# Performance work log

Hardware: AMD Instinct MI355X
Metric: run time of the kernel (lower is better)

## Reference

```python
import jax, jax.numpy as jnp
import numpy as np
import math

SEQ_LEN, PRED_LEN, CHANNELS, RANK = 720, 336, 862, 32
IN_LEN = SEQ_LEN // 2  # Haar low-pass with stride 2 (seq_len even)
BATCH = 256


def _dct2_ortho_mat(N):
    # D[k, n] = s_k * 2 * cos(pi * k * (2n+1) / (2N)); orthonormal DCT-II
    k = np.arange(N)[:, None]
    n = np.arange(N)[None, :]
    D = 2.0 * np.cos(np.pi * k * (2 * n + 1) / (2 * N))
    s = np.full(N, np.sqrt(1.0 / (2 * N)))
    s[0] = np.sqrt(1.0 / (4 * N))
    return jnp.asarray((s[:, None] * D).astype(np.float32))


def _idct2_unnorm_mat(N):
    # scipy.fft.idct(type=2, norm=None): out[n] = (1/N) * (x0/2 + sum_{k>=1} x_k cos(pi k (2n+1)/(2N)))
    # Returned as M[k, n] so that out = x @ M along last axis.
    k = np.arange(N)[:, None]
    n = np.arange(N)[None, :]
    M = np.cos(np.pi * k * (2 * n + 1) / (2 * N)) / N
    M[0, :] *= 0.5
    return jnp.asarray(M.astype(np.float32))


D_DCT = _dct2_ortho_mat(IN_LEN)        # [IN_LEN, IN_LEN]
M_IDCT = _idct2_unnorm_mat(PRED_LEN)   # [PRED_LEN, PRED_LEN]
INV_SQRT2 = 1.0 / math.sqrt(2.0)


def setup_inputs() -> dict:
    key = jax.random.key(0)
    k1, k2, k3, k4 = jax.random.split(key, 4)
    x = jax.random.normal(k1, (BATCH, SEQ_LEN, CHANNELS), dtype=jnp.float32)
    # kaiming_uniform-like scales for LowRank params
    boundA = math.sqrt(6.0 / IN_LEN)
    boundB = math.sqrt(6.0 / RANK)
    A = jax.random.uniform(k2, (IN_LEN, RANK), dtype=jnp.float32, minval=-boundA, maxval=boundA)
    B = jax.random.uniform(k3, (RANK, PRED_LEN), dtype=jnp.float32, minval=-boundB, maxval=boundB)
    b = jax.random.uniform(k4, (PRED_LEN,), dtype=jnp.float32)
    return {"x": x, "A": A, "B": B, "b": b}


def reference(x, A, B, b):
    # x: [B, L, C] -> [B, C, L]
    xt = jnp.transpose(x, (0, 2, 1))
    seq_mean = jnp.mean(xt, axis=-1, keepdims=True)          # [B, C, 1]
    xc = xt - seq_mean
    # Haar low-pass: depthwise conv1d with [1,1]/sqrt(2), stride 2
    h = (xc[..., ::2] + xc[..., 1::2]) * INV_SQRT2           # [B, C, IN_LEN]
    # orthonormal DCT-II along last axis, then divide by length
    y = jnp.einsum('bcn,kn->bck', h, D_DCT) / IN_LEN         # [B, C, IN_LEN]
    # low-rank prediction head (shared across channels)
    z = (y @ A) @ B + b                                      # [B, C, PRED_LEN]
    # unnormalized inverse DCT-II (scipy idct type=2, norm=None)
    o = z @ M_IDCT                                           # [B, C, PRED_LEN]
    o = o + seq_mean
    return jnp.transpose(o, (0, 2, 1))                       # [B, PRED_LEN, C]
```

## Files before the change

kernel.cpp:

```cpp
#include <hip/hip_runtime.h>
#include <math.h>

#define SEQ_LEN   720
#define IN_LEN    360
#define PRED_LEN  336
#define CHANNELS  862
#define RANK      32
#define BATCH     256

typedef _Float16 h2 __attribute__((ext_vector_type(2)));

#define WS_WP    0
#define WS_VT    11520
#define WS_CVEC  22272
#define WS_WH    22608
#define WS_VH    28368

__device__ __forceinline__ float fdot2w(h2 a, h2 b, float c) {
#if __has_builtin(__builtin_amdgcn_fdot2)
    return __builtin_amdgcn_fdot2(a, b, c, false);
#else
    return fmaf((float)a[0], (float)b[0], fmaf((float)a[1], (float)b[1], c));
#endif
}
__device__ __forceinline__ h2 pkrtz(float a, float b) {
    return __builtin_bit_cast(h2, __builtin_amdgcn_cvt_pkrtz(a, b));
}
#define BC(u) __builtin_bit_cast(h2, (u))

__global__ __launch_bounds__(256) void k_prep(const float* __restrict__ A,
                                              const float* __restrict__ B,
                                              const float* __restrict__ bias,
                                              float* __restrict__ Wp,
                                              float* __restrict__ Vt,
                                              float* __restrict__ cvec) {
    __shared__ float sbuf[IN_LEN * RANK];
    int blk = blockIdx.x;
    if (blk < 45) {
        for (int i = threadIdx.x; i < IN_LEN * RANK; i += 256) sbuf[i] = A[i];
        __syncthreads();
        int idx = blk * 256 + threadIdx.x;
        int n = idx >> 5, r = idx & 31;
        int step = 2 * n + 1, m = 0;
        float sum = 0.f;
        for (int k = 0; k < IN_LEN; ++k) {
            float coef = (k == 0) ? 0.05270462766947299f
                                  : 0.07453559924999299f;
            float d = coef * cospif((float)m * (1.0f / 720.0f));
            sum = fmaf(d, sbuf[k * RANK + r], sum);
            m += step; if (m >= 1440) m -= 1440;
        }
        Wp[idx] = sum * 0.0019641855032960957f;
    } else if (blk < 87) {
        for (int i = threadIdx.x; i < PRED_LEN * RANK; i += 256) {
            int r = i / PRED_LEN, k = i - r * PRED_LEN;
            sbuf[k * RANK + r] = B[i];
        }
        __syncthreads();
        int idx = (blk - 45) * 256 + threadIdx.x;
        int n = idx >> 5, r = idx & 31;
        int step = 2 * n + 1, m = 0;
        float sum = 0.f;
        for (int k = 0; k < PRED_LEN; ++k) {
            float mk = cospif((float)m * (1.0f / 672.0f));
            if (k == 0) mk *= 0.5f;
            sum = fmaf(mk, sbuf[k * RANK + r], sum);
            m += step; if (m >= 1344) m -= 1344;
        }
        Vt[idx] = sum * (1.0f / 336.0f);
    } else {
        int n = (blk - 87) * 256 + threadIdx.x;
        if (n < PRED_LEN) {
            int step = 2 * n + 1, m = 0;
            float sum = 0.f;
            for (int k = 0; k < PRED_LEN; ++k) {
                float mk = cospif((float)m * (1.0f / 672.0f));
                if (k == 0) mk *= 0.5f;
                sum = fmaf(mk, bias[k], sum);
                m += step; if (m >= 1344) m -= 1344;
            }
            cvec[n] = sum * (1.0f / 336.0f);
        }
    }
}

__global__ __launch_bounds__(256) void k_pack(const float* __restrict__ Wp,
                                              const float* __restrict__ Vt,
                                              unsigned* __restrict__ Wh,
                                              unsigned* __restrict__ Vh) {
    int idx = blockIdx.x * 256 + threadIdx.x;
    if (idx < 5760) {
        int np = idx >> 5, r = idx & 31;
        h2 v = pkrtz(Wp[(2 * np) * RANK + r], Wp[(2 * np + 1) * RANK + r]);
        Wh[idx] = __builtin_bit_cast(unsigned, v);
    } else if (idx < 5760 + 5376) {
        int j = idx - 5760;
        int n = j >> 4, q = j & 15;
        h2 v = pkrtz(Vt[n * RANK + 2 * q], Vt[n * RANK + 2 * q + 1]);
        Vh[j] = __builtin_bit_cast(unsigned, v);
    }
}

__global__ __launch_bounds__(256) void k_main(const float* __restrict__ x,
                                              const float* __restrict__ A,
                                              const unsigned* __restrict__ Wh,
                                              const unsigned* __restrict__ Vh,
                                              const float* __restrict__ cvec,
                                              float* __restrict__ out) {
    __shared__ uint4 lds4[1440];
    unsigned* ldsu = (unsigned*)lds4;
    const int tid = threadIdx.x;
    const int b = blockIdx.y;
    const int c = blockIdx.x * 256 + tid;
    const bool active = (c < CHANNELS);

    {
        const uint4* s = (const uint4*)Wh;
        for (int i = tid; i < 1440; i += 256) lds4[i] = s[i];
    }
    __syncthreads();

    float acc[RANK];
    #pragma unroll
    for (int r = 0; r < RANK; ++r) acc[r] = 0.f;
    float S = 0.f, mean = 0.f;
    h2 th[16];

    if (active) {
        const float* xp = x + (size_t)b * (SEQ_LEN * CHANNELS) + c;

        float bufA[8], bufB[8];
        #define LOADB(BUF, BD) { const float* p_ = xp + (size_t)(BD) * (8 * CHANNELS); \
            _Pragma("unroll") \
            for (int j_ = 0; j_ < 8; ++j_) BUF[j_] = p_[j_ * CHANNELS]; }

        #define NPBODY(BUF, S_) { \
            float pe = BUF[4*S_+0] + BUF[4*S_+1]; \
            float po = BUF[4*S_+2] + BUF[4*S_+3]; \
            S += pe + po; \
            h2 P = pkrtz(pe, po); \
            _Pragma("unroll") \
            for (int q_ = 0; q_ < 8; ++q_) { \
                uint4 wv = wr[8*S_ + q_]; \
                acc[4*q_+0] = fdot2w(P, BC(wv.x), acc[4*q_+0]); \
                acc[4*q_+1] = fdot2w(P, BC(wv.y), acc[4*q_+1]); \
                acc[4*q_+2] = fdot2w(P, BC(wv.z), acc[4*q_+2]); \
                acc[4*q_+3] = fdot2w(P, BC(wv.w), acc[4*q_+3]); \
            } }

        #define BODY(BUF, BD) { const uint4* wr = lds4 + 16 * (BD); \
            NPBODY(BUF, 0); NPBODY(BUF, 1); }

        LOADB(bufA, 0)
        for (int it = 0; it < 45; ++it) {
            LOADB(bufB, 2 * it + 1)
            BODY(bufA, 2 * it)
            if (it < 44) LOADB(bufA, 2 * it + 2)
            BODY(bufB, 2 * it + 1)
        }
        #undef BODY
        #undef NPBODY
        #undef LOADB

        const float k360 = (1.0f / 360.0f) * 0.037267799624996496f;
        float g = -S * k360;
        #pragma unroll
        for (int q = 0; q < 8; ++q) {
            float4 a4 = ((const float4*)A)[q];
            acc[4*q+0] = fmaf(g, a4.x, acc[4*q+0]);
            acc[4*q+1] = fmaf(g, a4.y, acc[4*q+1]);
            acc[4*q+2] = fmaf(g, a4.z, acc[4*q+2]);
            acc[4*q+3] = fmaf(g, a4.w, acc[4*q+3]);
        }
        mean = S * (1.0f / 720.0f);

        #pragma unroll
        for (int u = 0; u < 16; ++u) th[u] = pkrtz(acc[2*u], acc[2*u+1]);
    }
    __syncthreads();

    {
        const uint4* s = (const uint4*)Vh;
        for (int i = tid; i < 1344; i += 256) lds4[i] = s[i];
        for (int i = tid; i < PRED_LEN; i += 256)
            ldsu[5376 + i] = __float_as_uint(cvec[i]);
    }
    __syncthreads();

    if (active) {
        float* op = out + (size_t)b * (PRED_LEN * CHANNELS) + c;
        #pragma unroll 2
        for (int n = 0; n < PRED_LEN; ++n) {
            const uint4* vr = lds4 + n * 4;
            float oA = 0.f, oB = 0.f;
            #pragma unroll
            for (int q = 0; q < 4; ++q) {
                uint4 v = vr[q];
                oA = fdot2w(th[4*q+0], BC(v.x), oA);
                oB = fdot2w(th[4*q+1], BC(v.y), oB);
                oA = fdot2w(th[4*q+2], BC(v.z), oA);
                oB = fdot2w(th[4*q+3], BC(v.w), oB);
            }
            float cvn = __uint_as_float(ldsu[5376 + n]);
            *op = (oA + oB) + cvn + mean;
            op += CHANNELS;
        }
    }
}


extern "C" void kernel_launch(void* const* d_in, const int* in_sizes, int n_in,
                              void* d_out, int out_size, void* d_ws, size_t ws_size,
                              hipStream_t stream) {
    (void)in_sizes; (void)n_in; (void)out_size; (void)ws_size;
    const float* x    = (const float*)d_in[0];
    const float* A    = (const float*)d_in[1];
    const float* B    = (const float*)d_in[2];
    const float* bias = (const float*)d_in[3];
    float* out = (float*)d_out;
    float* ws  = (float*)d_ws;

    float*    Wp   = ws + WS_WP;
    float*    Vt   = ws + WS_VT;
    float*    cvec = ws + WS_CVEC;
    unsigned* Wh   = (unsigned*)(ws + WS_WH);
    unsigned* Vh   = (unsigned*)(ws + WS_VH);

    k_prep<<<dim3(89), dim3(256), 0, stream>>>(A, B, bias, Wp, Vt, cvec);
    k_pack<<<dim3(44), dim3(256), 0, stream>>>(Wp, Vt, Wh, Vh);
    k_main<<<dim3(4, BATCH), dim3(256), 0, stream>>>(x, A, Wh, Vh, cvec, out);
}
```

Measured before the change: 309.8 us.

## Process four channels per thread with packed-half FMA and split sequence halves

Restructures k_main so each of 512 threads handles four adjacent channels with float2 loads, and the two thread halves split the time axis in the projection phase and the output axis in the reconstruction phase. Partial accumulators are exchanged through LDS. Accumulation now uses packed fp16 FMA with fp16 accumulators instead of fdot2 into fp32, which raises throughput but risks precision loss over 180 accumulations. One block now covers a whole batch, with W, V and cvec staged in LDS once, cutting grid size and LDS reload overhead.

After: 271.6 us. -12.3%, faster.

```diff
diff --git a/kernel.cpp b/kernel.cpp
--- a/kernel.cpp
+++ b/kernel.cpp
@@ -16,6 +16,11 @@
 #define WS_WH    22608
 #define WS_VH    28368
 
+#define L_EX     0
+#define L_W      29376
+#define L_V      35136
+#define L_CV     40512
+
 __device__ __forceinline__ float fdot2w(h2 a, h2 b, float c) {
 #if __has_builtin(__builtin_amdgcn_fdot2)
     return __builtin_amdgcn_fdot2(a, b, c, false);
@@ -26,7 +31,8 @@
 __device__ __forceinline__ h2 pkrtz(float a, float b) {
     return __builtin_bit_cast(h2, __builtin_amdgcn_cvt_pkrtz(a, b));
 }
-#define BC(u) __builtin_bit_cast(h2, (u))
+#define BC(u)  __builtin_bit_cast(h2, (u))
+#define BCU(v) __builtin_bit_cast(unsigned, (v))
 
 __global__ __launch_bounds__(256) void k_prep(const float* __restrict__ A,
                                               const float* __restrict__ B,
@@ -90,119 +96,189 @@
                                               unsigned* __restrict__ Vh) {
     int idx = blockIdx.x * 256 + threadIdx.x;
     if (idx < 5760) {
-        int np = idx >> 5, r = idx & 31;
-        h2 v = pkrtz(Wp[(2 * np) * RANK + r], Wp[(2 * np + 1) * RANK + r]);
-        Wh[idx] = __builtin_bit_cast(unsigned, v);
+        int n = idx >> 4, j = idx & 15;
+        h2 v = pkrtz(Wp[n * RANK + 2 * j], Wp[n * RANK + 2 * j + 1]);
+        Wh[idx] = BCU(v);
     } else if (idx < 5760 + 5376) {
-        int j = idx - 5760;
-        int n = j >> 4, q = j & 15;
-        h2 v = pkrtz(Vt[n * RANK + 2 * q], Vt[n * RANK + 2 * q + 1]);
-        Vh[j] = __builtin_bit_cast(unsigned, v);
-    }
-}
-
-__global__ __launch_bounds__(256) void k_main(const float* __restrict__ x,
+        int k = idx - 5760;
+        int n = k >> 4, j = k & 15;
+        h2 v = pkrtz(Vt[n * RANK + 2 * j], Vt[n * RANK + 2 * j + 1]);
+        Vh[k] = BCU(v);
+    }
+}
+
+__global__ __launch_bounds__(512) void k_main(const float* __restrict__ x,
                                               const float* __restrict__ A,
                                               const unsigned* __restrict__ Wh,
                                               const unsigned* __restrict__ Vh,
                                               const float* __restrict__ cvec,
                                               float* __restrict__ out) {
-    __shared__ uint4 lds4[1440];
-    unsigned* ldsu = (unsigned*)lds4;
+    __shared__ unsigned ldsu[40848];
     const int tid = threadIdx.x;
-    const int b = blockIdx.y;
-    const int c = blockIdx.x * 256 + tid;
-    const bool active = (c < CHANNELS);
-
-    {
-        const uint4* s = (const uint4*)Wh;
-        for (int i = tid; i < 1440; i += 256) lds4[i] = s[i];
-    }
+    const int b = blockIdx.x;
+    const int h = tid >> 8;
+    const int i = tid & 255;
+    const bool active = (i < 216);
+    const int c0 = (i < 215) ? 4 * i : 858;
+
+    for (int idx = tid; idx < 1440; idx += 512)
+        ((uint4*)(ldsu + L_W))[idx] = ((const uint4*)Wh)[idx];
+    for (int idx = tid; idx < 1344; idx += 512)
+        ((uint4*)(ldsu + L_V))[idx] = ((const uint4*)Vh)[idx];
+    for (int idx = tid; idx < 84; idx += 512)
+        ((uint4*)(ldsu + L_CV))[idx] = ((const uint4*)cvec)[idx];
     __syncthreads();
 
-    float acc[RANK];
+    h2 acc0[16], acc1[16], acc2[16], acc3[16];
     #pragma unroll
-    for (int r = 0; r < RANK; ++r) acc[r] = 0.f;
-    float S = 0.f, mean = 0.f;
-    h2 th[16];
+    for (int j = 0; j < 16; ++j) {
+        acc0[j] = pkrtz(0.f, 0.f); acc1[j] = pkrtz(0.f, 0.f);
+        acc2[j] = pkrtz(0.f, 0.f); acc3[j] = pkrtz(0.f, 0.f);
+    }
+    float S0 = 0.f, S1 = 0.f, S2 = 0.f, S3 = 0.f;
 
     if (active) {
-        const float* xp = x + (size_t)b * (SEQ_LEN * CHANNELS) + c;
-
-        float bufA[8], bufB[8];
-        #define LOADB(BUF, BD) { const float* p_ = xp + (size_t)(BD) * (8 * CHANNELS); \
+        const float* xp = x + (size_t)b * (SEQ_LEN * CHANNELS)
+                            + (size_t)h * (IN_LEN * CHANNELS) + c0;
+        float2 bA[4], bB[4];
+        #define LOADN(BUF, NL) { const float* p_ = xp + (size_t)(2 * (NL)) * CHANNELS; \
+            BUF[0] = *(const float2*)(p_);                 \
+            BUF[1] = *(const float2*)(p_ + 2);             \
+            BUF[2] = *(const float2*)(p_ + CHANNELS);      \
+            BUF[3] = *(const float2*)(p_ + CHANNELS + 2); }
+
+        #define BODY(BUF, NL) { \
+            float p0 = BUF[0].x + BUF[2].x; \
+            float p1 = BUF[0].y + BUF[2].y; \
+            float p2 = BUF[1].x + BUF[3].x; \
+            float p3 = BUF[1].y + BUF[3].y; \
+            S0 += p0; S1 += p1; S2 += p2; S3 += p3; \
+            h2 P0 = pkrtz(p0, p0), P1 = pkrtz(p1, p1); \
+            h2 P2 = pkrtz(p2, p2), P3 = pkrtz(p3, p3); \
+            const uint4* wr = (const uint4*)(ldsu + L_W) + ((NL) + 180 * h) * 4; \
             _Pragma("unroll") \
-            for (int j_ = 0; j_ < 8; ++j_) BUF[j_] = p_[j_ * CHANNELS]; }
-
-        #define NPBODY(BUF, S_) { \
-            float pe = BUF[4*S_+0] + BUF[4*S_+1]; \
-            float po = BUF[4*S_+2] + BUF[4*S_+3]; \
-            S += pe + po; \
-            h2 P = pkrtz(pe, po); \
-            _Pragma("unroll") \
-            for (int q_ = 0; q_ < 8; ++q_) { \
-                uint4 wv = wr[8*S_ + q_]; \
-                acc[4*q_+0] = fdot2w(P, BC(wv.x), acc[4*q_+0]); \
-                acc[4*q_+1] = fdot2w(P, BC(wv.y), acc[4*q_+1]); \
-                acc[4*q_+2] = fdot2w(P, BC(wv.z), acc[4*q_+2]); \
-                acc[4*q_+3] = fdot2w(P, BC(wv.w), acc[4*q_+3]); \
+            for (int q_ = 0; q_ < 4; ++q_) { \
+                uint4 wv = wr[q_]; \
+                h2 w0 = BC(wv.x), w1 = BC(wv.y), w2 = BC(wv.z), w3 = BC(wv.w); \
+                acc0[4*q_+0] = w0 * P0 + acc0[4*q_+0]; \
+                acc1[4*q_+0] = w0 * P1 + acc1[4*q_+0]; \
+                acc2[4*q_+0] = w0 * P2 + acc2[4*q_+0]; \
+                acc3[4*q_+0] = w0 * P3 + acc3[4*q_+0]; \
+                acc0[4*q_+1] = w1 * P0 + acc0[4*q_+1]; \
+                acc1[4*q_+1] = w1 * P1 + acc1[4*q_+1]; \
+                acc2[4*q_+1] = w1 * P2 + acc2[4*q_+1]; \
+                acc3[4*q_+1] = w1 * P3 + acc3[4*q_+1]; \
+                acc0[4*q_+2] = w2 * P0 + acc0[4*q_+2]; \
+                acc1[4*q_+2] = w2 * P1 + acc1[4*q_+2]; \
+                acc2[4*q_+2] = w2 * P2 + acc2[4*q_+2]; \
+                acc3[4*q_+2] = w2 * P3 + acc3[4*q_+2]; \
+                acc0[4*q_+3] = w3 * P0 + acc0[4*q_+3]; \
+                acc1[4*q_+3] = w3 * P1 + acc1[4*q_+3]; \
+                acc2[4*q_+3] = w3 * P2 + acc2[4*q_+3]; \
+                acc3[4*q_+3] = w3 * P3 + acc3[4*q_+3]; \
             } }
 
-        #define BODY(BUF, BD) { const uint4* wr = lds4 + 16 * (BD); \
-            NPBODY(BUF, 0); NPBODY(BUF, 1); }
-
-        LOADB(bufA, 0)
-        for (int it = 0; it < 45; ++it) {
-            LOADB(bufB, 2 * it + 1)
-            BODY(bufA, 2 * it)
-            if (it < 44) LOADB(bufA, 2 * it + 2)
-            BODY(bufB, 2 * it + 1)
+        LOADN(bA, 0)
+        for (int n = 0; n < 180; n += 2) {
+            LOADN(bB, n + 1)
+            BODY(bA, n)
+            if (n + 2 < 180) LOADN(bA, n + 2)
+            BODY(bB, n + 1)
         }
         #undef BODY
-        #undef NPBODY
-        #undef LOADB
-
-        const float k360 = (1.0f / 360.0f) * 0.037267799624996496f;
-        float g = -S * k360;
+        #undef LOADN
+    }
+
+    if (active) {
+        uint4* rec = (uint4*)(ldsu + (i + 216 * h) * 68);
+        #pragma unroll
+        for (int q = 0; q < 4; ++q) {
+            uint4 v;
+            v.x = BCU(acc0[4*q+0]); v.y = BCU(acc0[4*q+1]);
+            v.z = BCU(acc0[4*q+2]); v.w = BCU(acc0[4*q+3]);
+            rec[q] = v;
+            v.x = BCU(acc1[4*q+0]); v.y = BCU(acc1[4*q+1]);
+            v.z = BCU(acc1[4*q+2]); v.w = BCU(acc1[4*q+3]);
+            rec[4 + q] = v;
+            v.x = BCU(acc2[4*q+0]); v.y = BCU(acc2[4*q+1]);
+            v.z = BCU(acc2[4*q+2]); v.w = BCU(acc2[4*q+3]);
+            rec[8 + q] = v;
+            v.x = BCU(acc3[4*q+0]); v.y = BCU(acc3[4*q+1]);
+            v.z = BCU(acc3[4*q+2]); v.w = BCU(acc3[4*q+3]);
+            rec[12 + q] = v;
+        }
+        uint4 sv;
+        sv.x = __float_as_uint(S0); sv.y = __float_as_uint(S1);
+        sv.z = __float_as_uint(S2); sv.w = __float_as_uint(S3);
+        rec[16] = sv;
+    }
+    __syncthreads();
+
+    float mean0 = 0.f, mean1 = 0.f, mean2 = 0.f, mean3 = 0.f;
+    if (active) {
+        const uint4* pr = (const uint4*)(ldsu + (i + 216 * (1 - h)) * 68);
+        #pragma unroll
+        for (int q = 0; q < 4; ++q) {
+            uint4 v = pr[q];
+            acc0[4*q+0] = acc0[4*q+0] + BC(v.x); acc0[4*q+1] = acc0[4*q+1] + BC(v.y);
+            acc0[4*q+2] = acc0[4*q+2] + BC(v.z); acc0[4*q+3] = acc0[4*q+3] + BC(v.w);
+            v = pr[4 + q];
+            acc1[4*q+0] = acc1[4*q+0] + BC(v.x); acc1[4*q+1] = acc1[4*q+1] + BC(v.y);
+            acc1[4*q+2] = acc1[4*q+2] + BC(v.z); acc1[4*q+3] = acc1[4*q+3] + BC(v.w);
+            v = pr[8 + q];
+            acc2[4*q+0] = acc2[4*q+0] + BC(v.x); acc2[4*q+1] = acc2[4*q+1] + BC(v.y);
+            acc2[4*q+2] = acc2[4*q+2] + BC(v.z); acc2[4*q+3] = acc2[4*q+3] + BC(v.w);
+            v = pr[12 + q];
+            acc3[4*q+0] = acc3[4*q+0] + BC(v.x); acc3[4*q+1] = acc3[4*q+1] + BC(v.y);
+            acc3[4*q+2] = acc3[4*q+2] + BC(v.z); acc3[4*q+3] = acc3[4*q+3] + BC(v.w);
+        }
+        uint4 sv = pr[16];
+        S0 += __uint_as_float(sv.x); S1 += __uint_as_float(sv.y);
+        S2 += __uint_as_float(sv.z); S3 += __uint_as_float(sv.w);
+
+        const float kc = (1.0f / 360.0f) * 0.037267799624996496f;
+        float g0 = -S0 * kc, g1 = -S1 * kc, g2 = -S2 * kc, g3 = -S3 * kc;
+        h2 G0 = pkrtz(g0, g0), G1 = pkrtz(g1, g1), G2 = pkrtz(g2, g2), G3 = pkrtz(g3, g3);
         #pragma unroll
         for (int q = 0; q < 8; ++q) {
             float4 a4 = ((const float4*)A)[q];
-            acc[4*q+0] = fmaf(g, a4.x, acc[4*q+0]);
-            acc[4*q+1] = fmaf(g, a4.y, acc[4*q+1]);
-            acc[4*q+2] = fmaf(g, a4.z, acc[4*q+2]);
-            acc[4*q+3] = fmaf(g, a4.w, acc[4*q+3]);
-        }
-        mean = S * (1.0f / 720.0f);
-
-        #pragma unroll
-        for (int u = 0; u < 16; ++u) th[u] = pkrtz(acc[2*u], acc[2*u+1]);
-    }
-    __syncthreads();
-
-    {
-        const uint4* s = (const uint4*)Vh;
-        for (int i = tid; i < 1344; i += 256) lds4[i] = s[i];
-        for (int i = tid; i < PRED_LEN; i += 256)
-            ldsu[5376 + i] = __float_as_uint(cvec[i]);
-    }
-    __syncthreads();
-
-    if (active) {
-        float* op = out + (size_t)b * (PRED_LEN * CHANNELS) + c;
-        #pragma unroll 2
-        for (int n = 0; n < PRED_LEN; ++n) {
-            const uint4* vr = lds4 + n * 4;
-            float oA = 0.f, oB = 0.f;
+            h2 aa = pkrtz(a4.x, a4.y), ab = pkrtz(a4.z, a4.w);
+            acc0[2*q]   = aa * G0 + acc0[2*q];   acc0[2*q+1] = ab * G0 + acc0[2*q+1];
+            acc1[2*q]   = aa * G1 + acc1[2*q];   acc1[2*q+1] = ab * G1 + acc1[2*q+1];
+            acc2[2*q]   = aa * G2 + acc2[2*q];   acc2[2*q+1] = ab * G2 + acc2[2*q+1];
+            acc3[2*q]   = aa * G3 + acc3[2*q];   acc3[2*q+1] = ab * G3 + acc3[2*q+1];
+        }
+        mean0 = S0 * (1.0f / 720.0f); mean1 = S1 * (1.0f / 720.0f);
+        mean2 = S2 * (1.0f / 720.0f); mean3 = S3 * (1.0f / 720.0f);
+
+        float* op = out + (size_t)b * (PRED_LEN * CHANNELS)
+                        + (size_t)(168 * h) * CHANNELS + c0;
+        for (int nl = 0; nl < 168; ++nl) {
+            const int n = 168 * h + nl;
+            const uint4* vr = (const uint4*)(ldsu + L_V) + n * 4;
+            float o0 = 0.f, o1 = 0.f, o2 = 0.f, o3 = 0.f;
+            float e0 = 0.f, e1 = 0.f, e2 = 0.f, e3 = 0.f;
             #pragma unroll
             for (int q = 0; q < 4; ++q) {
                 uint4 v = vr[q];
-                oA = fdot2w(th[4*q+0], BC(v.x), oA);
-                oB = fdot2w(th[4*q+1], BC(v.y), oB);
-                oA = fdot2w(th[4*q+2], BC(v.z), oA);
-                oB = fdot2w(th[4*q+3], BC(v.w), oB);
+                h2 v0 = BC(v.x), v1 = BC(v.y), v2 = BC(v.z), v3 = BC(v.w);
+                o0 = fdot2w(acc0[4*q+0], v0, o0); e0 = fdot2w(acc0[4*q+1], v1, e0);
+                o1 = fdot2w(acc1[4*q+0], v0, o1); e1 = fdot2w(acc1[4*q+1], v1, e1);
+                o2 = fdot2w(acc2[4*q+0], v0, o2); e2 = fdot2w(acc2[4*q+1], v1, e2);
+                o3 = fdot2w(acc3[4*q+0], v0, o3); e3 = fdot2w(acc3[4*q+1], v1, e3);
+                o0 = fdot2w(acc0[4*q+2], v2, o0); e0 = fdot2w(acc0[4*q+3], v3, e0);
+                o1 = fdot2w(acc1[4*q+2], v2, o1); e1 = fdot2w(acc1[4*q+3], v3, e1);
+                o2 = fdot2w(acc2[4*q+2], v2, o2); e2 = fdot2w(acc2[4*q+3], v3, e2);
+                o3 = fdot2w(acc3[4*q+2], v2, o3); e3 = fdot2w(acc3[4*q+3], v3, e3);
             }
-            float cvn = __uint_as_float(ldsu[5376 + n]);
-            *op = (oA + oB) + cvn + mean;
+            float cvn = ((const float*)(ldsu + L_CV))[n];
+            float2 w0, w1;
+            w0.x = (o0 + e0) + cvn + mean0;
+            w0.y = (o1 + e1) + cvn + mean1;
+            w1.x = (o2 + e2) + cvn + mean2;
+            w1.y = (o3 + e3) + cvn + mean3;
+            *(float2*)(op)     = w0;
+            *(float2*)(op + 2) = w1;
             op += CHANNELS;
         }
     }
@@ -228,5 +304,5 @@
 
     k_prep<<<dim3(89), dim3(256), 0, stream>>>(A, B, bias, Wp, Vt, cvec);
     k_pack<<<dim3(44), dim3(256), 0, stream>>>(Wp, Vt, Wh, Vh);
-    k_main<<<dim3(4, BATCH), dim3(256), 0, stream>>>(x, A, Wh, Vh, cvec, out);
-}
+    k_main<<<dim3(BATCH), dim3(512), 0, stream>>>(x, A, Wh, Vh, cvec, out);
+}
```
